# Kernel tuning notes

Measured on AMD Instinct MI355X. Metric: run time of the kernel, lower is better.

## Reference

```python
import jax, jax.numpy as jnp
import numpy as np

B, S, H, V, LLM_D, NL = 256, 200, 128, 50000, 768, 2
H2 = 2 * H
PAD_L = 256  # next power of two >= S
EPS = 1e-12


def _ln(x, g, b):
    mu = jnp.mean(x, axis=-1, keepdims=True)
    var = jnp.mean((x - mu) ** 2, axis=-1, keepdims=True)
    return (x - mu) / jnp.sqrt(var + EPS) * g + b


def _gelu(x):
    return jax.nn.gelu(x, approximate=False)


def _lru_scan(h, lamb0, mask):
    # Faithful recursive-doubling masked LRU scan.
    # h: [B, L, D] complex64; mask: [B, L] float32; lamb0: [1, D] complex64
    Bb, L, D = h.shape
    lamb = lamb0
    for i in range(1, int(np.log2(L)) + 1):
        l = 2 ** i
        h = h.reshape(Bb * L // l, l, D)
        m = mask.reshape(Bb * L // l, l)
        h1, h2 = h[:, : l // 2], h[:, l // 2 :]
        if i > 1:
            lamb = jnp.concatenate([lamb, lamb * lamb[-1]], axis=0)
        h2 = h2 + lamb * h1[:, -1:] * m[:, l // 2 - 1 : l // 2, None]
        h = jnp.concatenate([h1, h2], axis=1)
    return h.reshape(Bb, L, D)


def setup_inputs() -> dict:
    rng = np.random.default_rng(0)
    key = jax.random.key(0)
    ks = jax.random.split(key, 16)
    std = 0.02
    r_min, r_max = 0.8, 0.99
    # ring init of LRU diagonal (per layer)
    u1 = rng.uniform(size=(NL, H2)); u2 = rng.uniform(size=(NL, H2))
    nu_log = np.log(-0.5 * np.log(u1 * (r_max ** 2 - r_min ** 2) + r_min ** 2))
    theta_log = np.log(u2 * 2 * np.pi)
    diag = np.exp(-np.exp(nu_log) + 1j * np.exp(theta_log))
    gamma_log = np.log(np.sqrt(1 - np.abs(diag) ** 2))
    params_log = jnp.asarray(np.stack([nu_log, theta_log, gamma_log], axis=1), jnp.float32)  # [NL,3,H2]
    f32 = jnp.float32

    def rn(k, shape, s=std):
        return jax.random.normal(k, shape, f32) * s

    return dict(
        input_ids=jax.random.randint(ks[0], (B, S), 0, V),
        item_emb=rn(ks[1], (V, H)),
        llm_emb=rn(ks[2], (V, LLM_D), 1.0),
        W_map=rn(ks[3], (H, LLM_D)), b_map=jnp.zeros((H,), f32),
        Wg1=rn(ks[4], (2 * H, 2 * H)), bg1=jnp.zeros((2 * H,), f32),
        Wg2=rn(ks[5], (H, 2 * H)), bg2=jnp.zeros((H,), f32),
        ln0_g=jnp.ones((H,), f32), ln0_b=jnp.zeros((H,), f32),
        params_log=params_log,
        Win_re=rn(ks[6], (NL, H2, H)), Win_im=rn(ks[7], (NL, H2, H)),
        bin_re=jnp.zeros((NL, H2), f32), bin_im=jnp.zeros((NL, H2), f32),
        Wout_re=rn(ks[8], (NL, H, H2)), Wout_im=rn(ks[9], (NL, H, H2)),
        bout_re=jnp.zeros((NL, H), f32), bout_im=jnp.zeros((NL, H), f32),
        ln1_g=jnp.ones((NL, H), f32), ln1_b=jnp.zeros((NL, H), f32),
        Wff1=rn(ks[10], (NL, 4 * H, H)), bff1=jnp.zeros((NL, 4 * H), f32),
        Wff2=rn(ks[11], (NL, H, 4 * H)), bff2=jnp.zeros((NL, H), f32),
        ln2_g=jnp.ones((NL, H), f32), ln2_b=jnp.zeros((NL, H), f32),
    )


def reference(input_ids, item_emb, llm_emb, W_map, b_map, Wg1, bg1, Wg2, bg2,
              ln0_g, ln0_b, params_log, Win_re, Win_im, bin_re, bin_im,
              Wout_re, Wout_im, bout_re, bout_im, ln1_g, ln1_b,
              Wff1, bff1, Wff2, bff2, ln2_g, ln2_b):
    mask = input_ids > 0
    # dual embedding + dimension gating (dropout off in eval)
    ids = item_emb[input_ids]                              # [B,S,H]
    llm = llm_emb[input_ids] @ W_map.T + b_map             # [B,S,H]
    cat = jnp.concatenate([ids, llm], axis=-1)
    gate = jax.nn.sigmoid(_gelu(cat @ Wg1.T + bg1) @ Wg2.T + bg2)
    x = _ln(gate * ids + (1.0 - gate) * llm, ln0_g, ln0_b)
    pad = PAD_L - x.shape[1]
    x = jnp.pad(x, ((0, 0), (pad, 0), (0, 0)))             # left-pad seq dim
    m = jnp.pad(mask, ((0, 0), (pad, 0))).astype(jnp.float32)
    for l in range(NL):
        # --- LRU layer ---
        nu, theta, gamma = jnp.exp(params_log[l])          # each [H2]
        lamb0 = jnp.exp(-nu + 1j * theta)[None, :].astype(jnp.complex64)
        Win = (Win_re[l] + 1j * Win_im[l]).astype(jnp.complex64)
        bin_ = (bin_re[l] + 1j * bin_im[l]).astype(jnp.complex64)
        Wout = (Wout_re[l] + 1j * Wout_im[l]).astype(jnp.complex64)
        bout = (bout_re[l] + 1j * bout_im[l]).astype(jnp.complex64)
        h = (x.astype(jnp.complex64) @ Win.T + bin_) * gamma
        h = _lru_scan(h, lamb0, m)
        x = _ln((h @ Wout.T + bout).real + x, ln1_g[l], ln1_b[l])
        # --- position-wise FFN (Intermediate) ---
        ff = _gelu(x @ Wff1[l].T + bff1[l]) @ Wff2[l].T + bff2[l]
        x = _ln(ff + x, ln2_g[l], ln2_b[l])
    return x[:, -S:]
```

## Files before the change

kernel.cpp:

```cpp
#include <hip/hip_runtime.h>
#include <hip/hip_bf16.h>

#define CB 256
#define CS 200
#define CH 128
#define CH2 256
#define CL 256
#define CPAD 56
#define CBS (CB*CS)

typedef __attribute__((ext_vector_type(8))) short bf16x8;
typedef __attribute__((ext_vector_type(4))) float f32x4;

#define SB16 ((long)CBS*16)

__device__ __align__(16) __hip_bfloat16 g_cat [(size_t)CBS*256];
__device__ __align__(16) __hip_bfloat16 g_g1  [(size_t)CBS*256];
__device__ __align__(16) __hip_bfloat16 g_xb  [(size_t)CBS*128];
__device__ __align__(16) __hip_bfloat16 g_h   [(size_t)CBS*512];
__device__ __align__(16) __hip_bfloat16 g_ffh [(size_t)CBS*512];
__device__ float g_mask[CB*CL];
__device__ float g_gamma2[2*512];
__device__ float g_bincat[2*512];
__device__ float2 g_lam[2*16*128*16];
__device__ __align__(16) __hip_bfloat16 g_Wmap  [128*768];
__device__ __align__(16) __hip_bfloat16 g_Wg1   [256*256];
__device__ __align__(16) __hip_bfloat16 g_Wg2   [128*256];
__device__ __align__(16) __hip_bfloat16 g_Wincat[2*512*128];
__device__ __align__(16) __hip_bfloat16 g_Woutcat[2*128*512];
__device__ __align__(16) __hip_bfloat16 g_Wff1  [2*512*128];
__device__ __align__(16) __hip_bfloat16 g_Wff2  [2*128*512];

__device__ __forceinline__ short f2bf(float f){
  unsigned u = __float_as_uint(f);
  unsigned r = (u + 0x7fffu + ((u>>16)&1u)) >> 16;
  return (short)r;
}
__device__ __forceinline__ float bf2f(short s){
  return __uint_as_float(((unsigned)(unsigned short)s) << 16);
}

typedef const __attribute__((address_space(1))) void* gas1;
typedef __attribute__((address_space(3))) void* las3;
__device__ __forceinline__ void gl16(const void* g, void* l){
  __builtin_amdgcn_global_load_lds((gas1)g, (las3)l, 16, 0, 0);
}

__device__ __forceinline__ void wblk(__hip_bfloat16* dst, int N, int K, int i, float v){
  int r = i / K, c = i - r*K;
  ((short*)dst)[(long)(c>>4)*((long)N*16) + (long)r*16 + (c&15)] = f2bf(v);
}
__global__ void k_setup(const float* __restrict__ W_map, const float* __restrict__ Wg1,
                        const float* __restrict__ Wg2,
                        const float* __restrict__ Win_re, const float* __restrict__ Win_im,
                        const float* __restrict__ Wout_re, const float* __restrict__ Wout_im,
                        const float* __restrict__ Wff1, const float* __restrict__ Wff2,
                        const int* __restrict__ ids,
                        const float* __restrict__ pl,
                        const float* __restrict__ binre, const float* __restrict__ binim){
  int bi = blockIdx.x, t = threadIdx.x;
  if (bi < 2816){
    int i = bi*256 + t;
    if (i < 98304){ wblk(g_Wmap, 128, 768, i, W_map[i]); return; }
    i -= 98304;
    if (i < 65536){ wblk(g_Wg1, 256, 256, i, Wg1[i]); return; }
    i -= 65536;
    if (i < 32768){ wblk(g_Wg2, 128, 256, i, Wg2[i]); return; }
    i -= 32768;
    int l = i / 262144; i -= l*262144;
    if (i < 32768){ wblk(g_Wincat + (long)l*65536, 512, 128, i,       Win_re[(long)l*32768 + i]); return; }
    i -= 32768;
    if (i < 32768){ wblk(g_Wincat + (long)l*65536, 512, 128, i+32768, Win_im[(long)l*32768 + i]); return; }
    i -= 32768;
    if (i < 65536){
      int r = i >> 9, c = i & 511;
      float v = (c < 256) ? Wout_re[(long)l*32768 + r*256 + c]
                          : -Wout_im[(long)l*32768 + r*256 + (c-256)];
      wblk(g_Woutcat + (long)l*65536, 128, 512, i, v); return;
    }
    i -= 65536;
    if (i < 65536){ wblk(g_Wff1 + (long)l*65536, 512, 128, i, Wff1[(long)l*65536 + i]); return; }
    i -= 65536;
    wblk(g_Wff2 + (long)l*65536, 128, 512, i, Wff2[(long)l*65536 + i]);
    return;
  }
  if (bi < 3072){
    int b = bi - 2816;
    float m = 0.f;
    if (t >= CPAD) m = (ids[b*CS + (t - CPAD)] > 0) ? 1.f : 0.f;
    g_mask[b*CL + t] = m;
    return;
  }
  {
    int l = bi - 3072, d = t;
    float nu = expf(pl[(l*3+0)*CH2 + d]);
    float th = expf(pl[(l*3+1)*CH2 + d]);
    float gm = expf(pl[(l*3+2)*CH2 + d]);
    g_gamma2[l*512 + d] = gm;       g_gamma2[l*512 + d + 256] = gm;
    g_bincat[l*512 + d] = binre[l*256 + d];
    g_bincat[l*512 + d + 256] = binim[l*256 + d];
    float r = expf(-nu);
    float lre = r*cosf(th), lim = r*sinf(th);
    float pr = lre, pi = lim;
    long base = ((long)l*16 + (d>>4))*2048 + (d&15);
    for (int k = 0; k < 128; k++){
      g_lam[base + (long)k*16] = make_float2(pr, pi);
      float nr = pr*lre - pi*lim;
      float ni = pr*lim + pi*lre;
      pr = nr; pi = ni;
    }
  }
}

__global__ __launch_bounds__(256) void k_gather_ids(const int* __restrict__ ids,
                                                    const float* __restrict__ item_emb){
  int t = threadIdx.x;
  int tok = blockIdx.x*16 + (t>>4);
  int cg = t & 15;
  int id = ids[tok];
  const float* p = item_emb + (size_t)id*128 + cg*8;
  float4 x0 = *(const float4*)p;
  float4 x1 = *(const float4*)(p + 4);
  bf16x8 v;
  v[0]=f2bf(x0.x); v[1]=f2bf(x0.y); v[2]=f2bf(x0.z); v[3]=f2bf(x0.w);
  v[4]=f2bf(x1.x); v[5]=f2bf(x1.y); v[6]=f2bf(x1.z); v[7]=f2bf(x1.w);
  *(bf16x8*)((short*)g_cat + (long)(cg>>1)*SB16 + (long)tok*16 + (cg&1)*8) = v;
}

template<int TM, int ACT, int EPI, bool GATHER, bool COLSCALE>
__device__ __forceinline__ void mgemm_body(
    const short* __restrict__ A, const float* __restrict__ Af32, int ldaF,
    const short* __restrict__ W, long wBlk,
    const float* __restrict__ bias, const float* __restrict__ gamma,
    const int* __restrict__ gidx, short* __restrict__ C,
    long aBlk, int colOff, int K,
    const float* __restrict__ lnG, const float* __restrict__ lnB)
{
  constexpr int ACH = TM*32;
  __shared__ __align__(16) char lA[TM*128];
  __shared__ __align__(16) char lB[16384];
  constexpr int MF = (EPI==0) ? (TM/32) : 1;
  constexpr int NF = (EPI==0) ? 4 : 8;
  const int t = threadIdx.x;
  const int m0 = blockIdx.x*TM, n0 = blockIdx.y*128;
  const int lane = t & 63, wv = t >> 6;
  const int wr = (EPI==0)?(wv>>1):wv;
  const int wc = (EPI==0)?(wv&1):0;
  const int fr = lane & 15, fq = lane >> 4;
  const int rowB = (EPI==0) ? wr*(TM/2) : wv*16;
  const int colB = wc*64;

  long gr0 = 0, gr1 = 0;
  if (GATHER){ gr0 = gidx[m0 + (t>>3)]; gr1 = gidx[m0 + (t>>3) + 32]; }

  f32x4 acc[MF][NF] = {};

  for (int k0 = 0; k0 < K; k0 += 64){
    if (TM == 128){
      #pragma unroll
      for (int cc = 0; cc < 4; cc++){
        const short* gp = A + (long)((k0>>4)+cc)*aBlk + (long)(m0 + wv*32)*16 + (lane<<3);
        gl16(gp, lA + cc*4096 + wv*1024);
      }
      #pragma unroll
      for (int cc = 0; cc < 4; cc++){
        const short* gp = W + (long)((k0>>4)+cc)*wBlk + (long)(n0 + wv*32)*16 + (lane<<3);
        gl16(gp, lB + cc*4096 + wv*1024);
      }
    } else {
      if (GATHER){
        #pragma unroll
        for (int rep = 0; rep < 2; rep++){
          int slot = t + rep*256;
          int row = slot>>3, cc = (slot>>1)&3, half = slot&1;
          long ar = rep ? gr1 : gr0;
          const float* p = Af32 + ar*(long)ldaF + k0 + cc*16 + half*8;
          float4 x0 = *(const float4*)p;
          float4 x1 = *(const float4*)(p + 4);
          bf16x8 v;
          v[0]=f2bf(x0.x); v[1]=f2bf(x0.y); v[2]=f2bf(x0.z); v[3]=f2bf(x0.w);
          v[4]=f2bf(x1.x); v[5]=f2bf(x1.y); v[6]=f2bf(x1.z); v[7]=f2bf(x1.w);
          *(bf16x8*)(lA + cc*2048 + row*32 + half*16) = v;
        }
      } else {
        #pragma unroll
        for (int p = 0; p < 2; p++){
          const short* gp = A + (long)((k0>>4)+wv)*aBlk + (long)(m0 + p*32 + (lane>>1))*16 + (lane&1)*8;
          gl16(gp, lA + wv*2048 + p*1024);
        }
      }
      #pragma unroll
      for (int p = 0; p < 4; p++){
        const short* gp = W + (long)((k0>>4)+wv)*wBlk + (long)(n0 + p*32 + (lane>>1))*16 + (lane&1)*8;
        gl16(gp, lB + wv*4096 + p*1024);
      }
    }
    __syncthreads();
    #pragma unroll
    for (int s = 0; s < 2; s++){
      const int cc = s*2 + (fq>>1);
      bf16x8 af[MF], bw[NF];
      #pragma unroll
      for (int m = 0; m < MF; m++)
        af[m] = *(const bf16x8*)(lA + cc*ACH + (rowB + m*16 + fr)*32 + (fq&1)*16);
      #pragma unroll
      for (int n = 0; n < NF; n++)
        bw[n] = *(const bf16x8*)(lB + cc*4096 + (colB + n*16 + fr)*32 + (fq&1)*16);
      #pragma unroll
      for (int m = 0; m < MF; m++)
        #pragma unroll
        for (int n = 0; n < NF; n++)
          acc[m][n] = __builtin_amdgcn_mfma_f32_16x16x32_bf16(af[m], bw[n], acc[m][n], 0, 0, 0);
    }
    __syncthreads();
  }

  if (EPI == 0){
    #pragma unroll
    for (int m = 0; m < MF; m++){
      #pragma unroll
      for (int j = 0; j < 4; j++){
        long row = m0 + rowB + m*16 + fq*4 + j;
        #pragma unroll
        for (int n = 0; n < NF; n++){
          int colL = n0 + colB + n*16 + fr;
          float v = acc[m][n][j] + bias[colL];
          if (COLSCALE) v *= gamma[colL];
          if (ACT == 1) v = 0.5f * v * (1.0f + erff(v * 0.70710678118654752f));
          int colS = colL + colOff;
          C[(long)(colS>>4)*SB16 + row*16 + (colS&15)] = f2bf(v);
        }
      }
    }
  } else {
    #pragma unroll
    for (int j = 0; j < 4; j++){
      int rt = rowB + fq*4 + j;
      long tok = m0 + rt;
      float vv[NF];
      float s1 = 0.f, s2 = 0.f;
      #pragma unroll
      for (int n = 0; n < NF; n++){
        int col = n*16 + fr;
        float v = acc[0][n][j] + bias[col];
        if (EPI == 2){
          v = 1.0f / (1.0f + expf(-v));
          float idv = bf2f(((const short*)g_cat)[(long)n*SB16 + tok*16 + fr]);
          float lmv = bf2f(((const short*)g_cat)[(long)(n+8)*SB16 + tok*16 + fr]);
          v = v*idv + (1.0f - v)*lmv;
        } else {
          v += bf2f(((const short*)g_xb)[(long)n*SB16 + tok*16 + fr]);
        }
        vv[n] = v; s1 += v; s2 += v*v;
      }
      #pragma unroll
      for (int off = 1; off < 16; off <<= 1){
        s1 += __shfl_xor(s1, off); s2 += __shfl_xor(s2, off);
      }
      float mu = s1 * (1.f/128.f);
      float var = s2 * (1.f/128.f) - mu*mu;
      float rstd = rsqrtf(var + 1e-12f);
      #pragma unroll
      for (int n = 0; n < NF; n++){
        int col = n*16 + fr;
        float o = (vv[n] - mu)*rstd*lnG[col] + lnB[col];
        ((short*)g_xb)[(long)n*SB16 + tok*16 + fr] = f2bf(o);
      }
    }
  }
}

__global__ __launch_bounds__(256) void kg_llm(const float* llm_emb, const float* b_map, const int* ids){
  mgemm_body<64,0,0,true,false>(nullptr, llm_emb, 768, (const short*)g_Wmap, 128L*16,
                                b_map, nullptr, ids, (short*)g_cat, 0, 128, 768, nullptr, nullptr);
}
__global__ __launch_bounds__(256) void kg_g1(const float* bg1){
  mgemm_body<64,1,0,false,false>((const short*)g_cat, nullptr, 0, (const short*)g_Wg1, 256L*16,
                                 bg1, nullptr, nullptr, (short*)g_g1, SB16, 0, 256, nullptr, nullptr);
}
__global__ __launch_bounds__(256) void kg_gate(const float* bg2, const float* ln0g, const float* ln0b){
  mgemm_body<64,0,2,false,false>((const short*)g_g1, nullptr, 0, (const short*)g_Wg2, 128L*16,
                                 bg2, nullptr, nullptr, nullptr, SB16, 0, 256, ln0g, ln0b);
}
__global__ __launch_bounds__(256) void kg_h(int l){
  mgemm_body<128,0,0,false,true>((const short*)g_xb, nullptr, 0,
                                 (const short*)g_Wincat + (long)l*65536, 512L*16,
                                 g_bincat + l*512, g_gamma2 + l*512, nullptr, (short*)g_h,
                                 SB16, 0, 128, nullptr, nullptr);
}
__global__ __launch_bounds__(256) void kg_out(int l, const float* bout, const float* g, const float* b){
  mgemm_body<64,0,1,false,false>((const short*)g_h, nullptr, 0,
                                 (const short*)g_Woutcat + (long)l*65536, 128L*16,
                                 bout, nullptr, nullptr, nullptr, SB16, 0, 512, g, b);
}
__global__ __launch_bounds__(256) void kg_ff1(int l, const float* bff1){
  mgemm_body<128,1,0,false,false>((const short*)g_xb, nullptr, 0,
                                  (const short*)g_Wff1 + (long)l*65536, 512L*16,
                                  bff1, nullptr, nullptr, (short*)g_ffh, SB16, 0, 128, nullptr, nullptr);
}
__global__ __launch_bounds__(256) void kg_ff2(int l, const float* bff2, const float* g, const float* b){
  mgemm_body<64,0,1,false,false>((const short*)g_ffh, nullptr, 0,
                                 (const short*)g_Wff2 + (long)l*65536, 128L*16,
                                 bff2, nullptr, nullptr, nullptr, SB16, 0, 512, g, b);
}

__global__ __launch_bounds__(256) void k_scan(int l){
  __shared__ __align__(16) float sre[CL*16];
  __shared__ __align__(16) float sim[CL*16];
  __shared__ float smask[CL];
  int b = blockIdx.y, ch = blockIdx.x;
  int tid = threadIdx.x;
  short* Hre = (short*)g_h + (long)ch*SB16 + (long)b*CS*16;
  short* Him = (short*)g_h + (long)(ch+16)*SB16 + (long)b*CS*16;
  smask[tid] = g_mask[b*CL + tid];
  for (int q = tid; q < 224; q += 256){
    ((float4*)sre)[q] = make_float4(0.f,0.f,0.f,0.f);
    ((float4*)sim)[q] = make_float4(0.f,0.f,0.f,0.f);
  }
  for (int q = tid; q < 400; q += 256){
    bf16x8 r8 = ((const bf16x8*)Hre)[q];
    bf16x8 i8 = ((const bf16x8*)Him)[q];
    int base = 896 + q*8;
    #pragma unroll
    for (int k = 0; k < 8; k++){ sre[base+k] = bf2f(r8[k]); sim[base+k] = bf2f(i8[k]); }
  }
  __syncthreads();
  const float2* lam = g_lam + ((long)l*16 + ch)*2048;
  const int dl = tid & 15, u0 = tid >> 4;
  for (int i = 1; i <= 8; i++){
    int hl = 1 << (i-1);
    #pragma unroll
    for (int k = 0; k < 8; k++){
      int u = u0 + k*16;
      int blkI = u >> (i-1), j = u & (hl-1);
      int p = (blkI << i) + hl - 1;
      int tt = p + 1 + j;
      float mv = smask[p];
      float2 L = lam[j*16 + dl];
      float hr = sre[p*16+dl], hi = sim[p*16+dl];
      sre[tt*16+dl] += (L.x*hr - L.y*hi) * mv;
      sim[tt*16+dl] += (L.x*hi + L.y*hr) * mv;
    }
    __syncthreads();
  }
  for (int q = tid; q < 400; q += 256){
    int base = 896 + q*8;
    bf16x8 r8, i8;
    #pragma unroll
    for (int k = 0; k < 8; k++){ r8[k] = f2bf(sre[base+k]); i8[k] = f2bf(sim[base+k]); }
    ((bf16x8*)Hre)[q] = r8;
    ((bf16x8*)Him)[q] = i8;
  }
}

__global__ __launch_bounds__(256) void k_copy_out(float* __restrict__ out){
  int i = blockIdx.x*256 + threadIdx.x;
  int base = i*4;
  int tok = base >> 7, c = base & 127;
  short4 s4 = *(const short4*)((const short*)g_xb + (long)(c>>4)*SB16 + (long)tok*16 + (c&15));
  *(float4*)(out + base) = make_float4(bf2f(s4.x), bf2f(s4.y), bf2f(s4.z), bf2f(s4.w));
}

extern "C" void kernel_launch(void* const* d_in, const int* in_sizes, int n_in,
                              void* d_out, int out_size, void* d_ws, size_t ws_size,
                              hipStream_t stream) {
  const int*   ids       = (const int*)  d_in[0];
  const float* item_emb  = (const float*)d_in[1];
  const float* llm_emb   = (const float*)d_in[2];
  const float* W_map     = (const float*)d_in[3];
  const float* b_map     = (const float*)d_in[4];
  const float* Wg1       = (const float*)d_in[5];
  const float* bg1       = (const float*)d_in[6];
  const float* Wg2       = (const float*)d_in[7];
  const float* bg2       = (const float*)d_in[8];
  const float* ln0_g     = (const float*)d_in[9];
  const float* ln0_b     = (const float*)d_in[10];
  const float* params_log= (const float*)d_in[11];
  const float* Win_re    = (const float*)d_in[12];
  const float* Win_im    = (const float*)d_in[13];
  const float* bin_re    = (const float*)d_in[14];
  const float* bin_im    = (const float*)d_in[15];
  const float* Wout_re   = (const float*)d_in[16];
  const float* Wout_im   = (const float*)d_in[17];
  const float* bout_re   = (const float*)d_in[18];
  const float* ln1_g     = (const float*)d_in[20];
  const float* ln1_b     = (const float*)d_in[21];
  const float* Wff1      = (const float*)d_in[22];
  const float* bff1      = (const float*)d_in[23];
  const float* Wff2      = (const float*)d_in[24];
  const float* bff2      = (const float*)d_in[25];
  const float* ln2_g     = (const float*)d_in[26];
  const float* ln2_b     = (const float*)d_in[27];
  float* out = (float*)d_out;

  dim3 blk(256);

  k_setup<<<3074, blk, 0, stream>>>(W_map, Wg1, Wg2, Win_re, Win_im,
                                    Wout_re, Wout_im, Wff1, Wff2,
                                    ids, params_log, bin_re, bin_im);
  k_gather_ids<<<CBS/16, blk, 0, stream>>>(ids, item_emb);

  kg_llm <<<dim3(800,1), blk, 0, stream>>>(llm_emb, b_map, ids);
  kg_g1  <<<dim3(800,2), blk, 0, stream>>>(bg1);
  kg_gate<<<dim3(800,1), blk, 0, stream>>>(bg2, ln0_g, ln0_b);

  for (int l = 0; l < 2; l++){
    kg_h  <<<dim3(400,4), blk, 0, stream>>>(l);
    k_scan<<<dim3(16,CB), blk, 0, stream>>>(l);
    kg_out<<<dim3(800,1), blk, 0, stream>>>(l, bout_re + l*128, ln1_g + l*128, ln1_b + l*128);
    kg_ff1<<<dim3(400,4), blk, 0, stream>>>(l, bff1 + l*512);
    kg_ff2<<<dim3(800,1), blk, 0, stream>>>(l, bff2 + l*128, ln2_g + l*128, ln2_b + l*128);
  }

  k_copy_out<<<(CBS*CH)/1024, blk, 0, stream>>>(out);
}
```

Before: 440.2 us.

## Register-resident LRU scan, fuse gather into setup, write output from last FFN

Rewrites the LRU scan so each thread keeps its 16 timesteps in registers. Only the per-block carry values go through a small padded shared buffer, which removes the full sequence staging in LDS and the per-step lambda loads. Also folds the item embedding gather into the setup kernel. The final FFN2 layernorm epilogue now writes fp32 output directly, which drops the separate copy-out kernel and its extra pass over activations. Risks include higher register pressure in the scan and uncoalesced fp32 stores in the new epilogue.

```diff
diff --git a/kernel.cpp b/kernel.cpp
--- a/kernel.cpp
+++ b/kernel.cpp
@@ -57,7 +57,8 @@
                         const float* __restrict__ Wff1, const float* __restrict__ Wff2,
                         const int* __restrict__ ids,
                         const float* __restrict__ pl,
-                        const float* __restrict__ binre, const float* __restrict__ binim){
+                        const float* __restrict__ binre, const float* __restrict__ binim,
+                        const float* __restrict__ item_emb){
   int bi = blockIdx.x, t = threadIdx.x;
   if (bi < 2816){
     int i = bi*256 + t;
@@ -91,7 +92,7 @@
     g_mask[b*CL + t] = m;
     return;
   }
-  {
+  if (bi < 3074){
     int l = bi - 3072, d = t;
     float nu = expf(pl[(l*3+0)*CH2 + d]);
     float th = expf(pl[(l*3+1)*CH2 + d]);
@@ -109,22 +110,20 @@
       float ni = pr*lim + pi*lre;
       pr = nr; pi = ni;
     }
-  }
-}
-
-__global__ __launch_bounds__(256) void k_gather_ids(const int* __restrict__ ids,
-                                                    const float* __restrict__ item_emb){
-  int t = threadIdx.x;
-  int tok = blockIdx.x*16 + (t>>4);
-  int cg = t & 15;
-  int id = ids[tok];
-  const float* p = item_emb + (size_t)id*128 + cg*8;
-  float4 x0 = *(const float4*)p;
-  float4 x1 = *(const float4*)(p + 4);
-  bf16x8 v;
-  v[0]=f2bf(x0.x); v[1]=f2bf(x0.y); v[2]=f2bf(x0.z); v[3]=f2bf(x0.w);
-  v[4]=f2bf(x1.x); v[5]=f2bf(x1.y); v[6]=f2bf(x1.z); v[7]=f2bf(x1.w);
-  *(bf16x8*)((short*)g_cat + (long)(cg>>1)*SB16 + (long)tok*16 + (cg&1)*8) = v;
+    return;
+  }
+  {
+    int tok = (bi - 3074)*16 + (t>>4);
+    int cg = t & 15;
+    int id = ids[tok];
+    const float* p = item_emb + (size_t)id*128 + cg*8;
+    float4 x0 = *(const float4*)p;
+    float4 x1 = *(const float4*)(p + 4);
+    bf16x8 v;
+    v[0]=f2bf(x0.x); v[1]=f2bf(x0.y); v[2]=f2bf(x0.z); v[3]=f2bf(x0.w);
+    v[4]=f2bf(x1.x); v[5]=f2bf(x1.y); v[6]=f2bf(x1.z); v[7]=f2bf(x1.w);
+    *(bf16x8*)((short*)g_cat + (long)(cg>>1)*SB16 + (long)tok*16 + (cg&1)*8) = v;
+  }
 }
 
 template<int TM, int ACT, int EPI, bool GATHER, bool COLSCALE>
@@ -134,7 +133,8 @@
     const float* __restrict__ bias, const float* __restrict__ gamma,
     const int* __restrict__ gidx, short* __restrict__ C,
     long aBlk, int colOff, int K,
-    const float* __restrict__ lnG, const float* __restrict__ lnB)
+    const float* __restrict__ lnG, const float* __restrict__ lnB,
+    float* __restrict__ outF)
 {
   constexpr int ACH = TM*32;
   __shared__ __align__(16) char lA[TM*128];
@@ -264,7 +264,10 @@
       for (int n = 0; n < NF; n++){
         int col = n*16 + fr;
         float o = (vv[n] - mu)*rstd*lnG[col] + lnB[col];
-        ((short*)g_xb)[(long)n*SB16 + tok*16 + fr] = f2bf(o);
+        if (EPI == 3)
+          outF[tok*128 + col] = o;
+        else
+          ((short*)g_xb)[(long)n*SB16 + tok*16 + fr] = f2bf(o);
       }
     }
   }
@@ -272,93 +275,113 @@
 
 __global__ __launch_bounds__(256) void kg_llm(const float* llm_emb, const float* b_map, const int* ids){
   mgemm_body<64,0,0,true,false>(nullptr, llm_emb, 768, (const short*)g_Wmap, 128L*16,
-                                b_map, nullptr, ids, (short*)g_cat, 0, 128, 768, nullptr, nullptr);
+                                b_map, nullptr, ids, (short*)g_cat, 0, 128, 768, nullptr, nullptr, nullptr);
 }
 __global__ __launch_bounds__(256) void kg_g1(const float* bg1){
   mgemm_body<64,1,0,false,false>((const short*)g_cat, nullptr, 0, (const short*)g_Wg1, 256L*16,
-                                 bg1, nullptr, nullptr, (short*)g_g1, SB16, 0, 256, nullptr, nullptr);
+                                 bg1, nullptr, nullptr, (short*)g_g1, SB16, 0, 256, nullptr, nullptr, nullptr);
 }
 __global__ __launch_bounds__(256) void kg_gate(const float* bg2, const float* ln0g, const float* ln0b){
   mgemm_body<64,0,2,false,false>((const short*)g_g1, nullptr, 0, (const short*)g_Wg2, 128L*16,
-                                 bg2, nullptr, nullptr, nullptr, SB16, 0, 256, ln0g, ln0b);
+                                 bg2, nullptr, nullptr, nullptr, SB16, 0, 256, ln0g, ln0b, nullptr);
 }
 __global__ __launch_bounds__(256) void kg_h(int l){
   mgemm_body<128,0,0,false,true>((const short*)g_xb, nullptr, 0,
                                  (const short*)g_Wincat + (long)l*65536, 512L*16,
                                  g_bincat + l*512, g_gamma2 + l*512, nullptr, (short*)g_h,
-                                 SB16, 0, 128, nullptr, nullptr);
+                                 SB16, 0, 128, nullptr, nullptr, nullptr);
 }
 __global__ __launch_bounds__(256) void kg_out(int l, const float* bout, const float* g, const float* b){
   mgemm_body<64,0,1,false,false>((const short*)g_h, nullptr, 0,
                                  (const short*)g_Woutcat + (long)l*65536, 128L*16,
-                                 bout, nullptr, nullptr, nullptr, SB16, 0, 512, g, b);
+                                 bout, nullptr, nullptr, nullptr, SB16, 0, 512, g, b, nullptr);
 }
 __global__ __launch_bounds__(256) void kg_ff1(int l, const float* bff1){
   mgemm_body<128,1,0,false,false>((const short*)g_xb, nullptr, 0,
                                   (const short*)g_Wff1 + (long)l*65536, 512L*16,
-                                  bff1, nullptr, nullptr, (short*)g_ffh, SB16, 0, 128, nullptr, nullptr);
+                                  bff1, nullptr, nullptr, (short*)g_ffh, SB16, 0, 128, nullptr, nullptr, nullptr);
 }
 __global__ __launch_bounds__(256) void kg_ff2(int l, const float* bff2, const float* g, const float* b){
   mgemm_body<64,0,1,false,false>((const short*)g_ffh, nullptr, 0,
                                  (const short*)g_Wff2 + (long)l*65536, 128L*16,
-                                 bff2, nullptr, nullptr, nullptr, SB16, 0, 512, g, b);
+                                 bff2, nullptr, nullptr, nullptr, SB16, 0, 512, g, b, nullptr);
+}
+__global__ __launch_bounds__(256) void kg_ff2o(int l, const float* bff2, const float* g, const float* b,
+                                               float* outF){
+  mgemm_body<64,0,3,false,false>((const short*)g_ffh, nullptr, 0,
+                                 (const short*)g_Wff2 + (long)l*65536, 128L*16,
+                                 bff2, nullptr, nullptr, nullptr, SB16, 0, 512, g, b, outF);
 }
 
 __global__ __launch_bounds__(256) void k_scan(int l){
-  __shared__ __align__(16) float sre[CL*16];
-  __shared__ __align__(16) float sim[CL*16];
-  __shared__ float smask[CL];
-  int b = blockIdx.y, ch = blockIdx.x;
-  int tid = threadIdx.x;
+  __shared__ __align__(16) float2 cbuf[128*17];
+  const int b = blockIdx.y, ch = blockIdx.x;
+  const int tid = threadIdx.x, dl = tid & 15, g = tid >> 4;
   short* Hre = (short*)g_h + (long)ch*SB16 + (long)b*CS*16;
   short* Him = (short*)g_h + (long)(ch+16)*SB16 + (long)b*CS*16;
-  smask[tid] = g_mask[b*CL + tid];
-  for (int q = tid; q < 224; q += 256){
-    ((float4*)sre)[q] = make_float4(0.f,0.f,0.f,0.f);
-    ((float4*)sim)[q] = make_float4(0.f,0.f,0.f,0.f);
-  }
-  for (int q = tid; q < 400; q += 256){
-    bf16x8 r8 = ((const bf16x8*)Hre)[q];
-    bf16x8 i8 = ((const bf16x8*)Him)[q];
-    int base = 896 + q*8;
+  const float2* lam = g_lam + ((long)l*16 + ch)*2048;
+
+  float2 P[8];
+  #pragma unroll
+  for (int q = 0; q < 8; q++) P[q] = lam[(g + 16*q)*16 + dl];
+  float2 S1 = lam[0*16 + dl];
+  float2 S2 = lam[(g&1)*16 + dl];
+  float2 S3 = lam[(g&3)*16 + dl];
+  float2 S4 = lam[(g&7)*16 + dl];
+
+  unsigned mb = 0;
+  #pragma unroll
+  for (int k = 0; k < 16; k++){
+    int t = g + 16*k;
+    mb |= (g_mask[b*CL + t] != 0.f ? 1u : 0u) << k;
+  }
+
+  float2 h[16];
+  #pragma unroll
+  for (int k = 0; k < 16; k++){
+    int t = g + 16*k;
+    if (t >= CPAD){
+      int r = t - CPAD;
+      h[k].x = bf2f(Hre[r*16 + dl]);
+      h[k].y = bf2f(Him[r*16 + dl]);
+    } else { h[k].x = 0.f; h[k].y = 0.f; }
+  }
+
+  #pragma unroll
+  for (int i = 1; i <= 8; i++){
+    const int hl = 1 << (i-1);
     #pragma unroll
-    for (int k = 0; k < 8; k++){ sre[base+k] = bf2f(r8[k]); sim[base+k] = bf2f(i8[k]); }
-  }
-  __syncthreads();
-  const float2* lam = g_lam + ((long)l*16 + ch)*2048;
-  const int dl = tid & 15, u0 = tid >> 4;
-  for (int i = 1; i <= 8; i++){
-    int hl = 1 << (i-1);
+    for (int k = 0; k < 16; k++){
+      int t = g + 16*k;
+      if ((t & (2*hl-1)) == hl-1){
+        float m = ((mb >> k) & 1) ? 1.f : 0.f;
+        cbuf[(t>>i)*17 + dl] = make_float2(h[k].x*m, h[k].y*m);
+      }
+    }
+    __syncthreads();
     #pragma unroll
-    for (int k = 0; k < 8; k++){
-      int u = u0 + k*16;
-      int blkI = u >> (i-1), j = u & (hl-1);
-      int p = (blkI << i) + hl - 1;
-      int tt = p + 1 + j;
-      float mv = smask[p];
-      float2 L = lam[j*16 + dl];
-      float hr = sre[p*16+dl], hi = sim[p*16+dl];
-      sre[tt*16+dl] += (L.x*hr - L.y*hi) * mv;
-      sim[tt*16+dl] += (L.x*hi + L.y*hr) * mv;
+    for (int k = 0; k < 16; k++){
+      int t = g + 16*k;
+      if ((t >> (i-1)) & 1){
+        float2 cc = cbuf[(t>>i)*17 + dl];
+        float2 L = (i==1)?S1 : (i==2)?S2 : (i==3)?S3 : (i==4)?S4 :
+                   (i==5)?P[0] : (i==6)?P[k&1] : (i==7)?P[k&3] : P[k&7];
+        h[k].x += L.x*cc.x - L.y*cc.y;
+        h[k].y += L.x*cc.y + L.y*cc.x;
+      }
     }
     __syncthreads();
   }
-  for (int q = tid; q < 400; q += 256){
-    int base = 896 + q*8;
-    bf16x8 r8, i8;
-    #pragma unroll
-    for (int k = 0; k < 8; k++){ r8[k] = f2bf(sre[base+k]); i8[k] = f2bf(sim[base+k]); }
-    ((bf16x8*)Hre)[q] = r8;
-    ((bf16x8*)Him)[q] = i8;
-  }
-}
-
-__global__ __launch_bounds__(256) void k_copy_out(float* __restrict__ out){
-  int i = blockIdx.x*256 + threadIdx.x;
-  int base = i*4;
-  int tok = base >> 7, c = base & 127;
-  short4 s4 = *(const short4*)((const short*)g_xb + (long)(c>>4)*SB16 + (long)tok*16 + (c&15));
-  *(float4*)(out + base) = make_float4(bf2f(s4.x), bf2f(s4.y), bf2f(s4.z), bf2f(s4.w));
+
+  #pragma unroll
+  for (int k = 0; k < 16; k++){
+    int t = g + 16*k;
+    if (t >= CPAD){
+      int r = t - CPAD;
+      Hre[r*16 + dl] = f2bf(h[k].x);
+      Him[r*16 + dl] = f2bf(h[k].y);
+    }
+  }
 }
 
 extern "C" void kernel_launch(void* const* d_in, const int* in_sizes, int n_in,
@@ -395,10 +418,9 @@
 
   dim3 blk(256);
 
-  k_setup<<<3074, blk, 0, stream>>>(W_map, Wg1, Wg2, Win_re, Win_im,
+  k_setup<<<6274, blk, 0, stream>>>(W_map, Wg1, Wg2, Win_re, Win_im,
                                     Wout_re, Wout_im, Wff1, Wff2,
-                                    ids, params_log, bin_re, bin_im);
-  k_gather_ids<<<CBS/16, blk, 0, stream>>>(ids, item_emb);
+                                    ids, params_log, bin_re, bin_im, item_emb);
 
   kg_llm <<<dim3(800,1), blk, 0, stream>>>(llm_emb, b_map, ids);
   kg_g1  <<<dim3(800,2), blk, 0, stream>>>(bg1);
@@ -409,8 +431,9 @@
     k_scan<<<dim3(16,CB), blk, 0, stream>>>(l);
     kg_out<<<dim3(800,1), blk, 0, stream>>>(l, bout_re + l*128, ln1_g + l*128, ln1_b + l*128);
     kg_ff1<<<dim3(400,4), blk, 0, stream>>>(l, bff1 + l*512);
-    kg_ff2<<<dim3(800,1), blk, 0, stream>>>(l, bff2 + l*128, ln2_g + l*128, ln2_b + l*128);
-  }
-
-  k_copy_out<<<(CBS*CH)/1024, blk, 0, stream>>>(out);
-}
+    if (l == 0)
+      kg_ff2 <<<dim3(800,1), blk, 0, stream>>>(l, bff2 + l*128, ln2_g + l*128, ln2_b + l*128);
+    else
+      kg_ff2o<<<dim3(800,1), blk, 0, stream>>>(l, bff2 + l*128, ln2_g + l*128, ln2_b + l*128, out);
+  }
+}
```

New measurement: 463.5 us. 5.3% more time.
